# Kernel optimization log

Measured on AMD Instinct MI355X. Metric: run time of the kernel, lower is better.

Reference implementation:

```python
import jax, jax.numpy as jnp
import numpy as np
import math

B, S, E = 8, 1024, 1024
H, D = 8, 1024  # n_heads, d_q=d_k=d_v (must equal S and E per broadcasting in the original)


def setup_inputs() -> dict:
    key = jax.random.key(0)
    ks = jax.random.split(key, 9)
    sc_in = 1.0 / math.sqrt(E)
    inputs = jax.random.normal(ks[0], (B, S, E), dtype=jnp.float32)
    Wq = jax.random.uniform(ks[1], (E, H * D), jnp.float32, -sc_in, sc_in)
    bq = jax.random.uniform(ks[2], (H * D,), jnp.float32, -sc_in, sc_in)
    Wk = jax.random.uniform(ks[3], (E, H * D), jnp.float32, -sc_in, sc_in)
    bk = jax.random.uniform(ks[4], (H * D,), jnp.float32, -sc_in, sc_in)
    Wv = jax.random.uniform(ks[5], (E, H * D), jnp.float32, -sc_in, sc_in)
    bv = jax.random.uniform(ks[6], (H * D,), jnp.float32, -sc_in, sc_in)
    WL = jax.random.uniform(ks[7], (E, H * D), jnp.float32, -sc_in, sc_in)
    bL = jax.random.uniform(ks[8], (H * D,), jnp.float32, -sc_in, sc_in)
    return {"inputs": inputs, "Wq": Wq, "bq": bq, "Wk": Wk, "bk": bk,
            "Wv": Wv, "bv": bv, "WL": WL, "bL": bL}


def reference(inputs, Wq, bq, Wk, bk, Wv, bv, WL, bL):
    b = inputs.shape[0]
    # projections -> [B, H, S, D]
    def proj(W, bias):
        return (inputs @ W + bias).reshape(b, S, H, D).transpose(0, 2, 1, 3)
    q = proj(Wq, bq)
    k = proj(Wk, bk)
    v = proj(Wv, bv)
    # elementwise "kv" score: [B,H,S,D] * [B,H,D,S] (D==S so shapes align) -> [B,H,S,S]
    kv = k * jnp.swapaxes(v, -1, -2) * jnp.float32(1.0 / math.sqrt(D))
    attn = jax.nn.softmax(kv, axis=2)          # softmax over non-standard axis 2
    pooled = jnp.sum(attn * q, axis=2)         # [B, H, S]  (S == E)
    return pooled @ WL + bL                    # [B, H, H*D]
```

## Files before the change

kernel.cpp:

```cpp
#include <hip/hip_runtime.h>
#include <hip/hip_bf16.h>
#include <stdint.h>

typedef __attribute__((ext_vector_type(4))) float  f32x4;
typedef __attribute__((ext_vector_type(4))) float  fvec4;
typedef __attribute__((ext_vector_type(8))) short  bhalf8;
typedef __attribute__((ext_vector_type(4))) short  bhalf4;

typedef const __attribute__((address_space(1))) void glb_void;
typedef __attribute__((address_space(3))) void lds_void;

#define HD 8192
#define KDIM 1024

__device__ __forceinline__ float bf2f(short s) {
  union { float f; uint32_t u; } cv; cv.u = ((uint32_t)(uint16_t)s) << 16; return cv.f;
}
__device__ __forceinline__ short f2bf(float f) {
  union { float f; uint32_t u; } cv; cv.f = f;
  uint32_t u = cv.u;
  uint32_t r = (u + 0x7FFFu + ((u >> 16) & 1u)) >> 16;
  return (short)(uint16_t)r;
}

__global__ void cvt_f32_bf16(const float* __restrict__ in, short* __restrict__ out, int n8) {
  int idx = blockIdx.x * blockDim.x + threadIdx.x;
  if (idx >= n8) return;
  fvec4 a = ((const fvec4*)in)[idx * 2 + 0];
  fvec4 b = ((const fvec4*)in)[idx * 2 + 1];
  bhalf8 o;
  o[0]=f2bf(a[0]); o[1]=f2bf(a[1]); o[2]=f2bf(a[2]); o[3]=f2bf(a[3]);
  o[4]=f2bf(b[0]); o[5]=f2bf(b[1]); o[6]=f2bf(b[2]); o[7]=f2bf(b[3]);
  ((bhalf8*)out)[idx] = o;
}

__global__ __launch_bounds__(256)
void transpose_w(const float* __restrict__ W, short* __restrict__ WT) {
  __shared__ float tile[64][65];
  const int bk = blockIdx.x;
  const int bn = blockIdx.y;
  const int t  = threadIdx.x;
  #pragma unroll
  for (int p = 0; p < 4; ++p) {
    int r = p * 16 + (t >> 4);
    int c = (t & 15) * 4;
    fvec4 v = *(const fvec4*)(W + (size_t)(bk * 64 + r) * HD + bn * 64 + c);
    tile[r][c+0] = v[0]; tile[r][c+1] = v[1]; tile[r][c+2] = v[2]; tile[r][c+3] = v[3];
  }
  __syncthreads();
  #pragma unroll
  for (int p = 0; p < 2; ++p) {
    int rr = p * 32 + (t >> 3);
    int cc = (t & 7) * 8;
    bhalf8 o;
    #pragma unroll
    for (int e = 0; e < 8; ++e) o[e] = f2bf(tile[cc + e][rr]);
    *(bhalf8*)(WT + (size_t)(bn * 64 + rr) * KDIM + bk * 64 + cc) = o;
  }
}

#define BAR()  __builtin_amdgcn_s_barrier()
#define SBR()  __builtin_amdgcn_sched_barrier(0)
#define PRIO1  __builtin_amdgcn_s_setprio(1)
#define PRIO0  __builtin_amdgcn_s_setprio(0)

#define READ_A(DST, BUF, ROFF)                                                   \
  _Pragma("unroll") for (int mi = 0; mi < 4; ++mi)                               \
  _Pragma("unroll") for (int ks = 0; ks < 2; ++ks) {                             \
    int r_ = arow + (ROFF) + mi * 16;                                            \
    DST[mi][ks] = *(const bhalf8*)(smem + (BUF)*32768 + r_*64 +                  \
                                   (((ks*4 + kq) ^ (r_ & 7)) * 8)); }
#define READ_B(DST, BUF, ROFF)                                                   \
  _Pragma("unroll") for (int ni = 0; ni < 2; ++ni)                               \
  _Pragma("unroll") for (int ks = 0; ks < 2; ++ks) {                             \
    int r_ = brow + (ROFF) + ni * 16;                                            \
    DST[ni][ks] = *(const bhalf8*)(smem + (BUF)*32768 + 16384 + r_*64 +          \
                                   (((ks*4 + kq) ^ (r_ & 7)) * 8)); }
#define STAGE_A(BUF, H, KT)                                                      \
  _Pragma("unroll") for (int L_ = 0; L_ < 2; ++L_) {                             \
    __builtin_amdgcn_global_load_lds(                                            \
      (glb_void*)(Ag + (size_t)((H)*128 + (w*2 + L_)*8) * 1024 + (KT)),          \
      (lds_void*)((char*)smem + (BUF)*65536 + (H)*16384 + (w*2 + L_)*1024),      \
      16, 0, 0); }
#define STAGE_B(BUF, H, KT)                                                      \
  _Pragma("unroll") for (int L_ = 0; L_ < 2; ++L_) {                             \
    __builtin_amdgcn_global_load_lds(                                            \
      (glb_void*)(Bg + (size_t)((H)*128 + (w*2 + L_)*8) * 1024 + (KT)),          \
      (lds_void*)((char*)smem + (BUF)*65536 + 32768 + (H)*16384 + (w*2+L_)*1024),\
      16, 0, 0); }
#define MFMA_Q(MO, NO, AFR, BFR)                                                 \
  _Pragma("unroll") for (int mi = 0; mi < 4; ++mi)                               \
  _Pragma("unroll") for (int ni = 0; ni < 2; ++ni)                               \
  _Pragma("unroll") for (int ks = 0; ks < 2; ++ks)                               \
    acc[(MO)+mi][(NO)+ni] = __builtin_amdgcn_mfma_f32_16x16x32_bf16(             \
        AFR[mi][ks], BFR[ni][ks], acc[(MO)+mi][(NO)+ni], 0, 0, 0);

#define KTILE(BUF, DOSB, DOSA, KB, KA, VN) do {                                  \
  READ_A(a0, BUF, 0); READ_B(b0, BUF, 0);                                        \
  if (DOSB) { STAGE_B(BUF^1, 0, KB); }                                           \
  BAR(); SBR(); PRIO1; MFMA_Q(0, 0, a0, b0); PRIO0; SBR(); BAR();                \
  READ_A(a1, BUF, 64);                                                           \
  if (DOSB) { STAGE_B(BUF^1, 1, KB); }                                           \
  BAR(); SBR(); PRIO1; MFMA_Q(4, 0, a1, b0); PRIO0; SBR(); BAR();                \
  READ_B(b1, BUF, 32);                                                           \
  if (DOSA) { STAGE_A(BUF, 0, KA); }                                             \
  BAR(); SBR(); PRIO1; MFMA_Q(0, 2, a0, b1); PRIO0; SBR(); BAR();                \
  if (DOSA) { STAGE_A(BUF, 1, KA); }                                             \
  BAR(); SBR(); PRIO1; MFMA_Q(4, 2, a1, b1); PRIO0; SBR();                       \
  if ((VN) == 4)      asm volatile("s_waitcnt vmcnt(4)" ::: "memory");           \
  else if ((VN) == 0) asm volatile("s_waitcnt vmcnt(0)" ::: "memory");           \
  BAR();                                                                         \
} while (0)

template <bool TRANSPOSED>
__global__ __launch_bounds__(512, 2)
void gemm256(const short* __restrict__ A, const short* __restrict__ BT,
             const float* __restrict__ bias, short* __restrict__ C) {
  __shared__ alignas(16) short smem[65536];
  const int t    = threadIdx.x;
  const int lane = t & 63;
  const int w    = t >> 6;
  const int wr   = w >> 2, wc = w & 3;
  const int kq   = lane >> 4;

  const int nwg = gridDim.x;
  const int id  = blockIdx.x;
  const int wg  = (id & 7) * (nwg >> 3) + (id >> 3);
  const int bm  = wg >> 5;
  const int bn  = wg & 31;

  const int srow = lane >> 3;
  const int gk   = ((lane & 7) ^ srow) * 8;
  const short* Ag = A  + (size_t)(bm * 256 + srow) * 1024 + gk;
  const short* Bg = BT + (size_t)(bn * 256 + srow) * 1024 + gk;

  const int arow = wr * 128 + (lane & 15);
  const int brow = wc * 64  + (lane & 15);

  f32x4 acc[8][4];
  #pragma unroll
  for (int i = 0; i < 8; ++i)
    #pragma unroll
    for (int j = 0; j < 4; ++j) acc[i][j] = (f32x4)(0.f);
  bhalf8 a0[4][2], a1[4][2], b0[2][2], b1[2][2];

  STAGE_A(0, 0, 0);  STAGE_A(0, 1, 0);
  STAGE_B(0, 0, 0);  STAGE_B(0, 1, 0);
  STAGE_A(1, 0, 64); STAGE_A(1, 1, 64);
  asm volatile("s_waitcnt vmcnt(4)" ::: "memory");
  BAR();

  #pragma unroll 1
  for (int t2 = 0; t2 < 8; ++t2) {
    const bool more = (t2 < 7);
    KTILE(0, true, more, (2*t2 + 1) * 64, (2*t2 + 2) * 64, more ? 4 : 0);
    KTILE(1, more, more, (2*t2 + 2) * 64, (2*t2 + 3) * 64, more ? 4 : -1);
  }

  const int LDM = 264;
  if (TRANSPOSED) {
    const int bl   = bm >> 2;
    const int ioff = (bm & 3) * 256;
    #pragma unroll 1
    for (int p = 0; p < 2; ++p) {
      __syncthreads();
      if ((wc >> 1) == p) {
        #pragma unroll
        for (int ni = 0; ni < 4; ++ni) {
          float bb = bias[bn * 256 + wc * 64 + ni * 16 + (lane & 15)];
          int n128 = (wc & 1) * 64 + ni * 16 + (lane & 15);
          #pragma unroll
          for (int mi = 0; mi < 8; ++mi) {
            int mloc = wr * 128 + mi * 16 + kq * 4;
            bhalf4 pk;
            #pragma unroll
            for (int e = 0; e < 4; ++e) pk[e] = f2bf(acc[mi][ni][e] + bb);
            *(bhalf4*)(smem + n128 * LDM + mloc) = pk;
          }
        }
      }
      __syncthreads();
      #pragma unroll
      for (int r = 0; r < 4; ++r) {
        int row = r * 32 + (t >> 4);
        int ck  = (t & 15) * 16;
        bhalf8 v0 = *(const bhalf8*)(smem + row * LDM + ck);
        bhalf8 v1 = *(const bhalf8*)(smem + row * LDM + ck + 8);
        size_t dst = ((size_t)bl * HD + (bn * 256 + p * 128 + row)) * 1024 + ioff + ck;
        *(bhalf8*)(C + dst) = v0;
        *(bhalf8*)(C + dst + 8) = v1;
      }
    }
  } else {
    #pragma unroll 1
    for (int p = 0; p < 2; ++p) {
      __syncthreads();
      if (wr == p) {
        #pragma unroll
        for (int ni = 0; ni < 4; ++ni) {
          float bb = bias[bn * 256 + wc * 64 + ni * 16 + (lane & 15)];
          int nloc = wc * 64 + ni * 16 + (lane & 15);
          #pragma unroll
          for (int mi = 0; mi < 8; ++mi) {
            int mloc = mi * 16 + kq * 4;
            #pragma unroll
            for (int e = 0; e < 4; ++e)
              smem[(mloc + e) * LDM + nloc] = f2bf(acc[mi][ni][e] + bb);
          }
        }
      }
      __syncthreads();
      #pragma unroll
      for (int r = 0; r < 4; ++r) {
        int row = r * 32 + (t >> 4);
        int ck  = (t & 15) * 16;
        bhalf8 v0 = *(const bhalf8*)(smem + row * LDM + ck);
        bhalf8 v1 = *(const bhalf8*)(smem + row * LDM + ck + 8);
        size_t dst = (size_t)(bm * 256 + p * 128 + row) * HD + bn * 256 + ck;
        *(bhalf8*)(C + dst) = v0;
        *(bhalf8*)(C + dst + 8) = v1;
      }
    }
  }
}

template <bool TRANSPOSED>
__global__ __launch_bounds__(256, 2)
void gemm_proj(const short* __restrict__ A, const short* __restrict__ BT,
               const float* __restrict__ bias, short* __restrict__ C) {
  constexpr int LDC = 136;
  __shared__ alignas(16) short smem2[128 * LDC];
  short* As = smem2;
  short* Bs = smem2 + 8192;
  short* Cs = smem2;

  const int t    = threadIdx.x;
  const int lane = t & 63;
  const int wave = t >> 6;
  const int bm   = blockIdx.x >> 6;
  const int bn   = blockIdx.x & 63;
  const int wr   = wave >> 1, wc = wave & 1;

  f32x4 acc[4][4];
  #pragma unroll
  for (int i = 0; i < 4; ++i)
    #pragma unroll
    for (int j = 0; j < 4; ++j) acc[i][j] = (f32x4)(0.f);

  const int gslot = ((lane & 7) ^ (lane >> 3)) * 8;
  const short* aRow = A  + (size_t)(bm * 128 + (lane >> 3)) * KDIM + gslot;
  const short* bRow = BT + (size_t)(bn * 128 + (lane >> 3)) * KDIM + gslot;

  const int arow = wr * 64 + (lane & 15);
  const int brow = wc * 64 + (lane & 15);
  const int kbase = (lane >> 4) * 8;
  const int swz  = (lane & 7) * 8;

  for (int kt = 0; kt < 16; ++kt) {
    __syncthreads();
    #pragma unroll
    for (int s = 0; s < 4; ++s) {
      int c = s * 4 + wave;
      __builtin_amdgcn_global_load_lds(
          (glb_void*)(aRow + (size_t)(c * 8) * KDIM + kt * 64),
          (lds_void*)((char*)As + c * 1024), 16, 0, 0);
      __builtin_amdgcn_global_load_lds(
          (glb_void*)(bRow + (size_t)(c * 8) * KDIM + kt * 64),
          (lds_void*)((char*)Bs + c * 1024), 16, 0, 0);
    }
    __syncthreads();
    #pragma unroll
    for (int kk = 0; kk < 2; ++kk) {
      bhalf8 af[4], bfm[4];
      #pragma unroll
      for (int mi = 0; mi < 4; ++mi)
        af[mi] = *(const bhalf8*)(As + (arow + mi * 16) * 64 + ((kk * 32 + kbase) ^ swz));
      #pragma unroll
      for (int ni = 0; ni < 4; ++ni)
        bfm[ni] = *(const bhalf8*)(Bs + (brow + ni * 16) * 64 + ((kk * 32 + kbase) ^ swz));
      #pragma unroll
      for (int mi = 0; mi < 4; ++mi)
        #pragma unroll
        for (int ni = 0; ni < 4; ++ni)
          acc[mi][ni] = __builtin_amdgcn_mfma_f32_16x16x32_bf16(af[mi], bfm[ni], acc[mi][ni], 0, 0, 0);
    }
  }

  __syncthreads();

  float bv4[4];
  #pragma unroll
  for (int ni = 0; ni < 4; ++ni) bv4[ni] = bias[bn * 128 + wc * 64 + ni * 16 + (lane & 15)];

  #pragma unroll
  for (int mi = 0; mi < 4; ++mi) {
    #pragma unroll
    for (int ni = 0; ni < 4; ++ni) {
      const int r0 = wr * 64 + mi * 16 + (lane >> 4) * 4;
      const int cl = wc * 64 + ni * 16 + (lane & 15);
      if (TRANSPOSED) {
        bhalf4 pk;
        #pragma unroll
        for (int e = 0; e < 4; ++e) pk[e] = f2bf(acc[mi][ni][e] + bv4[ni]);
        *(bhalf4*)(Cs + cl * LDC + r0) = pk;
      } else {
        #pragma unroll
        for (int e = 0; e < 4; ++e) Cs[(r0 + e) * LDC + cl] = f2bf(acc[mi][ni][e] + bv4[ni]);
      }
    }
  }
  __syncthreads();

  #pragma unroll
  for (int p = 0; p < 8; ++p) {
    const int row = p * 16 + (t >> 4);
    const int ck  = (t & 15) * 8;
    bhalf8 v = *(const bhalf8*)(Cs + row * LDC + ck);
    if (TRANSPOSED) {
      const int n_g   = bn * 128 + row;
      const int mbase = bm * 128;
      const int bl    = mbase >> 10;
      const int ib    = (mbase & 1023) + ck;
      *(bhalf8*)(C + ((size_t)bl * HD + n_g) * 1024 + ib) = v;
    } else {
      const int m_g = bm * 128 + row;
      *(bhalf8*)(C + (size_t)m_g * HD + bn * 128 + ck) = v;
    }
  }
}

__global__ __launch_bounds__(256)
void pool_softmax(const short* __restrict__ QT, const short* __restrict__ KT,
                  const short* __restrict__ V, float* __restrict__ pooled, int b0) {
  const int t    = threadIdx.x;
  const int lane = t & 63;
  const int wave = t >> 6;
  const int task = blockIdx.x * 4 + wave;
  const int j  = task & 1023;
  const int bh = task >> 10;
  const int bl = bh >> 3, h = bh & 7;
  const size_t n = (size_t)h * 1024 + j;

  const bhalf8* qp = (const bhalf8*)(QT + ((size_t)bl * HD + n) * 1024);
  const bhalf8* kp = (const bhalf8*)(KT + ((size_t)bl * HD + n) * 1024);
  const bhalf8* vp = (const bhalf8*)(V + ((size_t)bl * 1024 + j) * HD + (size_t)h * 1024);

  bhalf8 q0 = qp[lane], q1 = qp[64 + lane];
  bhalf8 k0 = kp[lane], k1 = kp[64 + lane];
  bhalf8 v0 = vp[lane], v1 = vp[64 + lane];

  float q[16], x[16];
  float m = -1e30f;
  #pragma unroll
  for (int e = 0; e < 8; ++e) {
    q[e]     = bf2f(q0[e]);  q[8 + e] = bf2f(q1[e]);
    x[e]     = bf2f(k0[e]) * bf2f(v0[e]) * 0.03125f;
    x[8 + e] = bf2f(k1[e]) * bf2f(v1[e]) * 0.03125f;
  }
  #pragma unroll
  for (int e = 0; e < 16; ++e) m = fmaxf(m, x[e]);
  #pragma unroll
  for (int off = 32; off; off >>= 1) m = fmaxf(m, __shfl_xor(m, off, 64));
  float se = 0.f, sq = 0.f;
  #pragma unroll
  for (int e = 0; e < 16; ++e) { float ex = __expf(x[e] - m); se += ex; sq += ex * q[e]; }
  #pragma unroll
  for (int off = 32; off; off >>= 1) { se += __shfl_xor(se, off, 64); sq += __shfl_xor(sq, off, 64); }
  if (lane == 0) pooled[((size_t)(b0 * 8) + bh) * 1024 + j] = sq / se;
}

__global__ __launch_bounds__(256)
void final_gemm2(const float* __restrict__ pooled, const float* __restrict__ WL,
                 float* __restrict__ part) {
  __shared__ float sp[256][8];
  const int t  = threadIdx.x;
  const int bn = blockIdx.x;
  const int mg = blockIdx.y;
  const int kc = blockIdx.z;
  for (int idx = t; idx < 2048; idx += 256) {
    int mm = idx >> 8, k = idx & 255;
    sp[k][mm] = pooled[(size_t)(mg * 8 + mm) * 1024 + kc * 256 + k];
  }
  __syncthreads();
  const int n = bn * 256 + t;
  float acc[8];
  #pragma unroll
  for (int mm = 0; mm < 8; ++mm) acc[mm] = 0.f;
  const float* wp = WL + (size_t)(kc * 256) * HD + n;
  #pragma unroll 1
  for (int k0 = 0; k0 < 256; k0 += 8) {
    float wv[8];
    #pragma unroll
    for (int u = 0; u < 8; ++u) wv[u] = wp[(size_t)(k0 + u) * HD];
    #pragma unroll
    for (int u = 0; u < 8; ++u)
      #pragma unroll
      for (int mm = 0; mm < 8; ++mm) acc[mm] = fmaf(sp[k0 + u][mm], wv[u], acc[mm]);
  }
  #pragma unroll
  for (int mm = 0; mm < 8; ++mm)
    part[((size_t)kc * 64 + mg * 8 + mm) * HD + n] = acc[mm];
}

__global__ __launch_bounds__(256)
void final_reduce(const float* __restrict__ part, const float* __restrict__ bL,
                  float* __restrict__ out) {
  int id = blockIdx.x * 256 + threadIdx.x;
  const f32x4* p4 = (const f32x4*)part;
  f32x4 s = p4[id];
  s = s + p4[131072 + id];
  s = s + p4[262144 + id];
  s = s + p4[393216 + id];
  f32x4 bb = ((const f32x4*)bL)[id & 2047];
  ((f32x4*)out)[id] = s + bb;
}

extern "C" void kernel_launch(void* const* d_in, const int* in_sizes, int n_in,
                              void* d_out, int out_size, void* d_ws, size_t ws_size,
                              hipStream_t stream) {
  const float* inputs = (const float*)d_in[0];
  const float* Wq = (const float*)d_in[1];
  const float* bq = (const float*)d_in[2];
  const float* Wk = (const float*)d_in[3];
  const float* bk = (const float*)d_in[4];
  const float* Wv = (const float*)d_in[5];
  const float* bv = (const float*)d_in[6];
  const float* WL = (const float*)d_in[7];
  const float* bL = (const float*)d_in[8];
  float* out = (float*)d_out;

  const size_t MB = 1ull << 20;
  int CB; bool threeW;
  if      (ws_size >= 449 * MB) { CB = 8; threeW = true;  }
  else if (ws_size >= 249 * MB) { CB = 4; threeW = true;  }
  else if (ws_size >= 149 * MB) { CB = 2; threeW = true;  }
  else if (ws_size >=  99 * MB) { CB = 1; threeW = true;  }
  else                          { CB = 1; threeW = false; }

  char* ws = (char*)d_ws;
  short* WT0 = (short*)ws;
  short* WT1 = threeW ? (short*)(ws + 16 * MB) : WT0;
  short* WT2 = threeW ? (short*)(ws + 32 * MB) : WT0;
  char* pp = ws + (threeW ? 48 : 16) * MB;
  short* Abf = (short*)pp;  pp += (size_t)CB * 2  * MB;
  short* QT  = (short*)pp;  pp += (size_t)CB * 16 * MB;
  short* KT  = (short*)pp;  pp += (size_t)CB * 16 * MB;
  short* Vn  = (short*)pp;  pp += (size_t)CB * 16 * MB;
  float* pooled = (float*)pp;
  float* part = (float*)QT;

  const float* Wmat[3] = {Wq, Wk, Wv};
  const float* bvec[3] = {bq, bk, bv};
  short*       WTs[3]  = {WT0, WT1, WT2};
  short*       Cout[3] = {QT, KT, Vn};
  const bool   big = (CB >= 2);

  dim3 tg(16, 128);
  if (threeW)
    for (int pj = 0; pj < 3; ++pj)
      transpose_w<<<tg, 256, 0, stream>>>(Wmat[pj], WTs[pj]);

  for (int b0 = 0; b0 < 8; b0 += CB) {
    cvt_f32_bf16<<<CB * 512, 256, 0, stream>>>(inputs + ((size_t)b0 << 20), Abf, CB << 17);
    for (int pj = 0; pj < 3; ++pj) {
      if (!threeW)
        transpose_w<<<tg, 256, 0, stream>>>(Wmat[pj], WT0);
      if (big) {
        if (pj < 2)
          gemm256<true ><<<CB * 128, 512, 0, stream>>>(Abf, WTs[pj], bvec[pj], Cout[pj]);
        else
          gemm256<false><<<CB * 128, 512, 0, stream>>>(Abf, WTs[pj], bvec[pj], Cout[pj]);
      } else {
        if (pj < 2)
          gemm_proj<true ><<<CB * 512, 256, 0, stream>>>(Abf, WTs[pj], bvec[pj], Cout[pj]);
        else
          gemm_proj<false><<<CB * 512, 256, 0, stream>>>(Abf, WTs[pj], bvec[pj], Cout[pj]);
      }
    }
    pool_softmax<<<CB * 2048, 256, 0, stream>>>(QT, KT, Vn, pooled, b0);
  }
  final_gemm2<<<dim3(32, 8, 4), 256, 0, stream>>>(pooled, WL, part);
  final_reduce<<<512, 256, 0, stream>>>(part, bL, out);
}
```

Baseline: 599.0 us.

## Restructure GEMM k-loop pipeline to prefetch next-tile fragments and whole tiles

Replaces the KTILE macro with a new KT2 schedule that double-buffers both A and B tiles in LDS. Next-buffer register fragments are read during the last MFMA quarters, and sched_barriers and partial vmcnt waits are removed in favour of a single vmcnt(0) per tile. The workgroup-to-tile mapping also changes to a new blockIdx swizzle that groups blocks by N. The intent is to overlap LDS reads and global loads more fully with MFMA work, at the cost of a different barrier and wait placement that is more exposed to hazards and L2 locality changes.

```diff
diff --git a/kernel.cpp b/kernel.cpp
--- a/kernel.cpp
+++ b/kernel.cpp
@@ -60,7 +60,6 @@
 }
 
 #define BAR()  __builtin_amdgcn_s_barrier()
-#define SBR()  __builtin_amdgcn_sched_barrier(0)
 #define PRIO1  __builtin_amdgcn_s_setprio(1)
 #define PRIO0  __builtin_amdgcn_s_setprio(0)
 
@@ -95,21 +94,26 @@
     acc[(MO)+mi][(NO)+ni] = __builtin_amdgcn_mfma_f32_16x16x32_bf16(             \
         AFR[mi][ks], BFR[ni][ks], acc[(MO)+mi][(NO)+ni], 0, 0, 0);
 
-#define KTILE(BUF, DOSB, DOSA, KB, KA, VN) do {                                  \
-  READ_A(a0, BUF, 0); READ_B(b0, BUF, 0);                                        \
-  if (DOSB) { STAGE_B(BUF^1, 0, KB); }                                           \
-  BAR(); SBR(); PRIO1; MFMA_Q(0, 0, a0, b0); PRIO0; SBR(); BAR();                \
-  READ_A(a1, BUF, 64);                                                           \
-  if (DOSB) { STAGE_B(BUF^1, 1, KB); }                                           \
-  BAR(); SBR(); PRIO1; MFMA_Q(4, 0, a1, b0); PRIO0; SBR(); BAR();                \
-  READ_B(b1, BUF, 32);                                                           \
-  if (DOSA) { STAGE_A(BUF, 0, KA); }                                             \
-  BAR(); SBR(); PRIO1; MFMA_Q(0, 2, a0, b1); PRIO0; SBR(); BAR();                \
-  if (DOSA) { STAGE_A(BUF, 1, KA); }                                             \
-  BAR(); SBR(); PRIO1; MFMA_Q(4, 2, a1, b1); PRIO0; SBR();                       \
-  if ((VN) == 4)      asm volatile("s_waitcnt vmcnt(4)" ::: "memory");           \
-  else if ((VN) == 0) asm volatile("s_waitcnt vmcnt(0)" ::: "memory");           \
+#define KT2(B, DOST, DORD, KA) do {                                              \
+                                                                         \
   BAR();                                                                         \
+  READ_A(a1, B, 64);                                                             \
+  PRIO1; MFMA_Q(0, 0, a0, b0); PRIO0;                                            \
+                                                                         \
+  BAR();                                                                         \
+  READ_B(b1, B, 32);                                                             \
+  PRIO1; MFMA_Q(4, 0, a1, b0); PRIO0;                                            \
+  asm volatile("s_waitcnt vmcnt(0)" ::: "memory");                               \
+                                                                         \
+  BAR();                                                                         \
+  if (DOST) { STAGE_A(B, 0, KA); STAGE_A(B, 1, KA); }                            \
+  if (DORD) { READ_B(b0, (B)^1, 0); }                                            \
+  PRIO1; MFMA_Q(0, 2, a0, b1); PRIO0;                                            \
+                                                                         \
+  BAR();                                                                         \
+  if (DOST) { STAGE_B(B, 0, KA); STAGE_B(B, 1, KA); }                            \
+  if (DORD) { READ_A(a0, (B)^1, 0); }                                            \
+  PRIO1; MFMA_Q(4, 2, a1, b1); PRIO0;                                            \
 } while (0)
 
 template <bool TRANSPOSED>
@@ -123,11 +127,10 @@
   const int wr   = w >> 2, wc = w & 3;
   const int kq   = lane >> 4;
 
-  const int nwg = gridDim.x;
-  const int id  = blockIdx.x;
-  const int wg  = (id & 7) * (nwg >> 3) + (id >> 3);
-  const int bm  = wg >> 5;
-  const int bn  = wg & 31;
+  const int x  = blockIdx.x & 7;
+  const int s  = blockIdx.x >> 3;
+  const int bm = s >> 2;
+  const int bn = x * 4 + (s & 3);
 
   const int srow = lane >> 3;
   const int gk   = ((lane & 7) ^ srow) * 8;
@@ -144,18 +147,22 @@
     for (int j = 0; j < 4; ++j) acc[i][j] = (f32x4)(0.f);
   bhalf8 a0[4][2], a1[4][2], b0[2][2], b1[2][2];
 
-  STAGE_A(0, 0, 0);  STAGE_A(0, 1, 0);
-  STAGE_B(0, 0, 0);  STAGE_B(0, 1, 0);
-  STAGE_A(1, 0, 64); STAGE_A(1, 1, 64);
-  asm volatile("s_waitcnt vmcnt(4)" ::: "memory");
+  STAGE_A(0, 0, 0);   STAGE_A(0, 1, 0);
+  STAGE_B(0, 0, 0);   STAGE_B(0, 1, 0);
+  STAGE_A(1, 0, 64);  STAGE_A(1, 1, 64);
+  STAGE_B(1, 0, 64);  STAGE_B(1, 1, 64);
+  asm volatile("s_waitcnt vmcnt(8)" ::: "memory");
   BAR();
+  READ_A(a0, 0, 0);
+  READ_B(b0, 0, 0);
 
   #pragma unroll 1
-  for (int t2 = 0; t2 < 8; ++t2) {
-    const bool more = (t2 < 7);
-    KTILE(0, true, more, (2*t2 + 1) * 64, (2*t2 + 2) * 64, more ? 4 : 0);
-    KTILE(1, more, more, (2*t2 + 2) * 64, (2*t2 + 3) * 64, more ? 4 : -1);
-  }
+  for (int t2 = 0; t2 < 7; ++t2) {
+    KT2(0, 1, 1, (2 * t2 + 2) * 64);
+    KT2(1, 1, 1, (2 * t2 + 3) * 64);
+  }
+  KT2(0, 0, 1, 0);
+  KT2(1, 0, 0, 0);
 
   const int LDM = 264;
   if (TRANSPOSED) {
```

New measurement: 862.9 us. +44.1%, slower.
